# Performance work log

Hardware: AMD Instinct MI355X
Metric: run time of the kernel (lower is better)

The kernel has to match this reference:

```python
import jax, jax.numpy as jnp
import numpy as np

N = 100000   # nodes
E = 1600000  # edges (before self loops)
D = 128      # input_dim
H1 = 128     # hidden_dim_1
H2 = 128     # hidden_dim_2
OUT = 1      # output_dim
G = 64       # number of graphs in the batch


def setup_inputs() -> dict:
    key = jax.random.key(0)
    ks = jax.random.split(key, 11)
    x = jax.random.normal(ks[0], (N, D), dtype=jnp.float32)
    edge_index = jax.random.randint(ks[1], (2, E), 0, N, dtype=jnp.int64)
    batch = jnp.sort(jax.random.randint(ks[2], (N,), 0, G, dtype=jnp.int64))
    s = 0.05
    W1 = jax.random.normal(ks[3], (D, H1), dtype=jnp.float32) * s
    b1 = jnp.zeros((H1,), dtype=jnp.float32)
    W2 = jax.random.normal(ks[4], (H1, H2), dtype=jnp.float32) * s
    b2 = jnp.zeros((H2,), dtype=jnp.float32)
    W_iou = jax.random.normal(ks[5], (H2, OUT), dtype=jnp.float32) * s
    b_iou = jnp.zeros((OUT,), dtype=jnp.float32)
    W_iop = jax.random.normal(ks[6], (H2, OUT), dtype=jnp.float32) * s
    b_iop = jnp.zeros((OUT,), dtype=jnp.float32)
    return dict(x=x, edge_index=edge_index, batch=batch,
                W1=W1, b1=b1, W2=W2, b2=b2,
                W_iou=W_iou, b_iou=b_iou, W_iop=W_iop, b_iop=b_iop)


def reference(x, edge_index, batch, W1, b1, W2, b2, W_iou, b_iou, W_iop, b_iop):
    n = x.shape[0]
    # add_self_loops
    loops = jnp.arange(n, dtype=edge_index.dtype)
    src = jnp.concatenate([edge_index[0], loops])
    dst = jnp.concatenate([edge_index[1], loops])
    # symmetric GCN normalization: deg over target nodes
    deg = jax.ops.segment_sum(jnp.ones_like(dst, dtype=x.dtype), dst, num_segments=n)
    dinv = jnp.where(deg > 0, jax.lax.rsqrt(deg), 0.0)
    norm = dinv[src] * dinv[dst]  # [E+N]

    def gcn_conv(h, W, b):
        hw = h @ W                                  # [N, H]
        m = hw[src] * norm[:, None]                 # gather + normalize [E+N, H]
        return jax.ops.segment_sum(m, dst, num_segments=n) + b  # scatter-add

    h = jax.nn.relu(gcn_conv(x, W1, b1))
    h = jax.nn.relu(gcn_conv(h, W2, b2))
    # global_max_pool over graph ids
    pooled = jax.ops.segment_max(h, batch, num_segments=G)
    pooled = jnp.where(jnp.isfinite(pooled), pooled, 0.0)  # guard empty graphs
    iou = pooled @ W_iou + b_iou
    iop = pooled @ W_iop + b_iop
    return jnp.concatenate([iou, iop], axis=1)  # [G, 2*OUT]
```

## Files before the change

kernel.cpp:

```cpp
#include <hip/hip_runtime.h>
#include <math.h>

typedef unsigned int u32;
typedef __attribute__((ext_vector_type(8))) short short8v;
typedef __attribute__((ext_vector_type(4))) float floatx4;

__device__ inline int rfl(int v) { return __builtin_amdgcn_readfirstlane(v); }

__device__ inline float blo(u32 u) { return __uint_as_float(u << 16); }
__device__ inline float bhi(u32 u) { return __uint_as_float(u & 0xffff0000u); }
__device__ inline u32 f2b(float f) {
    u32 u = __float_as_uint(f);
    return (u + 0x7fffu + ((u >> 16) & 1u)) >> 16;
}
__device__ inline u32 pack2(float a, float b) { return f2b(a) | (f2b(b) << 16); }

#define FILL_EPT 16
__global__ __launch_bounds__(256) void bfill_k(const int* __restrict__ src, const int* __restrict__ dst,
                                               u32* __restrict__ gcursor, u32* __restrict__ pairs,
                                               int E, int B, int CAP) {
    __shared__ u32 lcnt[256];
    __shared__ u32 lbase[256];
    const int t = threadIdx.x;
    lcnt[t] = 0;
    __syncthreads();

    const int base_e = blockIdx.x * (256 * FILL_EPT);
    u32 pk[FILL_EPT];
    u32 bk[FILL_EPT];
    u32 rk[FILL_EPT];
#pragma unroll
    for (int q = 0; q < FILL_EPT / 4; ++q) {
        int e0 = base_e + (q * 256 + t) * 4;
        if (e0 + 3 < E) {
            int4 s4 = *(const int4*)(src + e0);
            int4 d4 = *(const int4*)(dst + e0);
            int ss[4] = {s4.x, s4.y, s4.z, s4.w};
            int dd[4] = {d4.x, d4.y, d4.z, d4.w};
#pragma unroll
            for (int r = 0; r < 4; ++r) {
                int j = q * 4 + r;
                u32 b = (u32)dd[r] >> 9;
                pk[j] = (u32)ss[r] | (((u32)dd[r] & 511u) << 17);
                bk[j] = b;
                rk[j] = atomicAdd(&lcnt[b], 1u);
            }
        } else {
#pragma unroll
            for (int r = 0; r < 4; ++r) {
                int j = q * 4 + r;
                int e = e0 + r;
                pk[j] = 0xFFFFFFFFu;
                if (e < E) {
                    int d = dst[e];
                    u32 b = (u32)d >> 9;
                    pk[j] = (u32)src[e] | (((u32)d & 511u) << 17);
                    bk[j] = b;
                    rk[j] = atomicAdd(&lcnt[b], 1u);
                }
            }
        }
    }
    __syncthreads();
    if (t < B) {
        u32 v = lcnt[t];
        lbase[t] = v ? atomicAdd(&gcursor[t], v) : 0u;
    }
    __syncthreads();
#pragma unroll
    for (int j = 0; j < FILL_EPT; ++j) {
        if (pk[j] != 0xFFFFFFFFu) {
            u32 b = bk[j];
            u32 pos = lbase[b] + rk[j];
            if (pos < (u32)CAP) pairs[(size_t)b * CAP + pos] = pk[j];
        }
    }
}

__global__ __launch_bounds__(512) void csort_k(const u32* __restrict__ pairs, const u32* __restrict__ gcursor,
                                               u32* __restrict__ csr, uint2* __restrict__ rowinfo,
                                               float* __restrict__ dinv, int N, int CAP,
                                               const float* __restrict__ W1, const float* __restrict__ W2,
                                               ushort* __restrict__ W1t, ushort* __restrict__ W2t,
                                               u32* __restrict__ pooled) {
    __shared__ u32 hist[512];
    __shared__ u32 scanb[512];
    const int b = blockIdx.x, t = threadIdx.x;
    const u32 base = (u32)b * (u32)CAP;
    u32 cnt = gcursor[b];
    if (cnt > (u32)CAP) cnt = (u32)CAP;

    hist[t] = 0u;
    __syncthreads();
    for (u32 j = t; j < cnt; j += 512) {
        u32 p = pairs[base + j];
        atomicAdd(&hist[p >> 17], 1u);
    }
    __syncthreads();
    u32 v = hist[t];
    scanb[t] = v;
    __syncthreads();
    for (int off = 1; off < 512; off <<= 1) {
        u32 x = (t >= off) ? scanb[t - off] : 0u;
        __syncthreads();
        scanb[t] += x;
        __syncthreads();
    }
    u32 excl_t = scanb[t] - v;

    int i = (b << 9) + t;
    if (i < N) {
        rowinfo[i] = make_uint2(base + excl_t, v);
        dinv[i] = rsqrtf((float)(v + 1u));
    }
    __syncthreads();
    hist[t] = excl_t;
    __syncthreads();
    for (u32 j = t; j < cnt; j += 512) {
        u32 p = pairs[base + j];
        u32 loc = p >> 17;
        u32 pos = atomicAdd(&hist[loc], 1u);
        csr[base + pos] = p & 0x1FFFFu;
    }

    if (b < 32) {
        int idx = b * 512 + t;
        int k = idx >> 7, jj = idx & 127;
        W1t[jj * 128 + k] = (ushort)f2b(W1[idx]);
        W2t[jj * 128 + k] = (ushort)f2b(W2[idx]);
    } else if (b < 48) {
        int idx = (b - 32) * 512 + t;
        pooled[idx] = 0u;
    }
}

__device__ inline int swz(int row, int kbyte) { return row * 256 + (kbyte ^ ((row & 7) << 4)); }

template <bool BF16IN>
__global__ __launch_bounds__(512) void gemm_mfma_k(const void* __restrict__ inp, const ushort* __restrict__ Wt,
                                                   const float* __restrict__ dinv,
                                                   ushort* __restrict__ outp, int N) {
    __shared__ char Wl[128 * 256];
    const int t = threadIdx.x;
    const int brow = blockIdx.x * 256;

    {
        const uint4* g = (const uint4*)Wt;
#pragma unroll
        for (int i = 0; i < 4; ++i) {
            int f = t + i * 512;
            int r = f >> 4, kb = (f & 15) << 4;
            *(uint4*)(Wl + swz(r, kb)) = g[f];
        }
    }

    const int lane = t & 63;
    const int wave = t >> 6;
    const int l15 = lane & 15;
    const int g4 = lane >> 4;

    short8v a[2][4];
#pragma unroll
    for (int mt = 0; mt < 2; ++mt) {
        int row = brow + wave * 32 + mt * 16 + l15;
        bool ok = row < N;
        int rowc = ok ? row : 0;
#pragma unroll
        for (int ks = 0; ks < 4; ++ks) {
            uint4 v = make_uint4(0u, 0u, 0u, 0u);
            if (BF16IN) {
                if (ok) v = *(const uint4*)((const char*)inp + (size_t)rowc * 256 + (ks * 64 + g4 * 16));
            } else {
                if (ok) {
                    const float4* p = (const float4*)((const char*)inp + (size_t)rowc * 512 + (ks * 128 + g4 * 32));
                    float4 x0 = p[0], x1 = p[1];
                    v = make_uint4(pack2(x0.x, x0.y), pack2(x0.z, x0.w), pack2(x1.x, x1.y), pack2(x1.z, x1.w));
                }
            }
            a[mt][ks] = *(short8v*)&v;
        }
    }
    __syncthreads();

    floatx4 acc[2][8];
#pragma unroll
    for (int mt = 0; mt < 2; ++mt)
#pragma unroll
        for (int nt = 0; nt < 8; ++nt) acc[mt][nt] = (floatx4){0.f, 0.f, 0.f, 0.f};

#pragma unroll
    for (int ks = 0; ks < 4; ++ks) {
        int kb = ks * 64 + g4 * 16;
        short8v b[8];
#pragma unroll
        for (int nt = 0; nt < 8; ++nt)
            b[nt] = *(const short8v*)(Wl + swz(nt * 16 + l15, kb));
#pragma unroll
        for (int mt = 0; mt < 2; ++mt)
#pragma unroll
            for (int nt = 0; nt < 8; ++nt)
                acc[mt][nt] = __builtin_amdgcn_mfma_f32_16x16x32_bf16(a[mt][ks], b[nt], acc[mt][nt], 0, 0, 0);
    }

    const int r0w = g4 * 4;
#pragma unroll
    for (int mt = 0; mt < 2; ++mt) {
#pragma unroll
        for (int reg = 0; reg < 4; ++reg) {
            int grow = brow + wave * 32 + mt * 16 + r0w + reg;
            if (grow < N) {
                float sc = dinv[grow];
#pragma unroll
                for (int nt = 0; nt < 8; ++nt)
                    outp[grow * 128 + nt * 16 + l15] = (ushort)f2b(acc[mt][nt][reg] * sc);
            }
        }
    }
}

__device__ inline void edge_row_accum8(const u32* __restrict__ hw, const u32* __restrict__ csr,
                                       int r0, int deg, int lane, float& a0, float& a1) {
    int j = 0;
    for (; j + 8 <= deg; j += 8) {
        int s0 = rfl((int)csr[r0 + j + 0]);
        int s1 = rfl((int)csr[r0 + j + 1]);
        int s2 = rfl((int)csr[r0 + j + 2]);
        int s3 = rfl((int)csr[r0 + j + 3]);
        int s4 = rfl((int)csr[r0 + j + 4]);
        int s5 = rfl((int)csr[r0 + j + 5]);
        int s6 = rfl((int)csr[r0 + j + 6]);
        int s7 = rfl((int)csr[r0 + j + 7]);
        u32 u0 = hw[(size_t)s0 * 64 + lane];
        u32 u1 = hw[(size_t)s1 * 64 + lane];
        u32 u2 = hw[(size_t)s2 * 64 + lane];
        u32 u3 = hw[(size_t)s3 * 64 + lane];
        u32 u4 = hw[(size_t)s4 * 64 + lane];
        u32 u5 = hw[(size_t)s5 * 64 + lane];
        u32 u6 = hw[(size_t)s6 * 64 + lane];
        u32 u7 = hw[(size_t)s7 * 64 + lane];
        a0 += blo(u0); a1 += bhi(u0);
        a0 += blo(u1); a1 += bhi(u1);
        a0 += blo(u2); a1 += bhi(u2);
        a0 += blo(u3); a1 += bhi(u3);
        a0 += blo(u4); a1 += bhi(u4);
        a0 += blo(u5); a1 += bhi(u5);
        a0 += blo(u6); a1 += bhi(u6);
        a0 += blo(u7); a1 += bhi(u7);
    }
    if (j < deg) {
        const int rem = deg - j;
#pragma unroll
        for (int k = 0; k < 8; ++k) {
            int off = (k < rem) ? k : (rem - 1);
            int s = rfl((int)csr[r0 + j + off]);
            u32 u = hw[(size_t)s * 64 + lane];
            float v0 = (k < rem) ? blo(u) : 0.f;
            float v1 = (k < rem) ? bhi(u) : 0.f;
            a0 += v0; a1 += v1;
        }
    }
}

__global__ __launch_bounds__(256) void edge_accum_k(const u32* __restrict__ hw, const uint2* __restrict__ rowinfo,
                                                    const u32* __restrict__ csr, const float* __restrict__ dinv,
                                                    const float* __restrict__ bias, u32* __restrict__ hout, int N) {
    const int lane = threadIdx.x & 63;
    const int wid = (blockIdx.x * blockDim.x + threadIdx.x) >> 6;
    const int nw = (gridDim.x * blockDim.x) >> 6;
    const float2 bb = ((const float2*)bias)[lane];

    for (int i = wid; i < N; i += nw) {
        uint2 ri = rowinfo[i];
        const int r0 = rfl((int)ri.x);
        const int deg = rfl((int)ri.y);
        float di = dinv[i];
        u32 us = hw[(size_t)i * 64 + lane];
        float a0 = blo(us), a1 = bhi(us);

        edge_row_accum8(hw, csr, r0, deg, lane, a0, a1);

        a0 = fmaxf(fmaf(a0, di, bb.x), 0.f);
        a1 = fmaxf(fmaf(a1, di, bb.y), 0.f);
        hout[(size_t)i * 64 + lane] = pack2(a0, a1);
    }
}

__global__ __launch_bounds__(256) void edge_pool_k(const u32* __restrict__ hw, const uint2* __restrict__ rowinfo,
                                                   const u32* __restrict__ csr, const float* __restrict__ dinv,
                                                   const float* __restrict__ bias, const int* __restrict__ batch,
                                                   u32* __restrict__ pooled, int N, int chunk) {
    const int lane = threadIdx.x & 63;
    const int gwid = (blockIdx.x * blockDim.x + threadIdx.x) >> 6;
    const float2 bb = ((const float2*)bias)[lane];

    int i0 = gwid * chunk, i1 = min(N, i0 + chunk);
    float m0 = 0.f, m1 = 0.f;
    int gcur = -1;
    for (int i = i0; i < i1; ++i) {
        uint2 ri = rowinfo[i];
        const int r0 = rfl((int)ri.x);
        const int deg = rfl((int)ri.y);
        float di = dinv[i];
        u32 us = hw[(size_t)i * 64 + lane];
        float a0 = blo(us), a1 = bhi(us);

        edge_row_accum8(hw, csr, r0, deg, lane, a0, a1);

        a0 = fmaxf(fmaf(a0, di, bb.x), 0.f);
        a1 = fmaxf(fmaf(a1, di, bb.y), 0.f);

        int g = batch[i];
        if (g != gcur) {
            if (gcur >= 0) {
                atomicMax(pooled + gcur * 128 + lane * 2,     __float_as_uint(m0));
                atomicMax(pooled + gcur * 128 + lane * 2 + 1, __float_as_uint(m1));
            }
            gcur = g;
            m0 = m1 = 0.f;
        }
        m0 = fmaxf(m0, a0);
        m1 = fmaxf(m1, a1);
    }
    if (gcur >= 0) {
        atomicMax(pooled + gcur * 128 + lane * 2,     __float_as_uint(m0));
        atomicMax(pooled + gcur * 128 + lane * 2 + 1, __float_as_uint(m1));
    }
}

__global__ void final_k(const float* __restrict__ pooled, const float* __restrict__ Wu, const float* __restrict__ bu,
                        const float* __restrict__ Wp, const float* __restrict__ bp, float* __restrict__ out) {
    int t = threadIdx.x;
    int g = t >> 1, c = t & 1;
    const float* w = c ? Wp : Wu;
    const float* pr = pooled + g * 128;
    float s = 0.f;
    for (int k = 0; k < 128; k += 4)
        s += pr[k] * w[k] + pr[k + 1] * w[k + 1] + pr[k + 2] * w[k + 2] + pr[k + 3] * w[k + 3];
    out[g * 2 + c] = s + (c ? bp[0] : bu[0]);
}

extern "C" void kernel_launch(void* const* d_in, const int* in_sizes, int n_in,
                              void* d_out, int out_size, void* d_ws, size_t ws_size,
                              hipStream_t stream) {
    const float* x     = (const float*)d_in[0];
    const int*   ei    = (const int*)d_in[1];
    const int*   batch = (const int*)d_in[2];
    const float* W1    = (const float*)d_in[3];
    const float* b1    = (const float*)d_in[4];
    const float* W2    = (const float*)d_in[5];
    const float* b2    = (const float*)d_in[6];
    const float* Wu    = (const float*)d_in[7];
    const float* bu    = (const float*)d_in[8];
    const float* Wp    = (const float*)d_in[9];
    const float* bp    = (const float*)d_in[10];
    float* out = (float*)d_out;

    const int N = in_sizes[2];
    const int E = in_sizes[1] / 2;
    const int* src = ei;
    const int* dst = ei + E;

    const int B = (N + 511) >> 9;
    int avg = E / B;
    int CAP = avg + 6 * (int)sqrt((double)avg) + 64;
    CAP = (CAP + 63) & ~63;

    char* ws = (char*)d_ws;
    size_t o = 0;
    auto alloc = [&](size_t bytes) { size_t r = o; o += (bytes + 255) & ~(size_t)255; return r; };
    u32*   gcursor = (u32*)(ws + alloc(1024));
    float* dinv    = (float*)(ws + alloc((size_t)N * 4));
    uint2* rowinfo = (uint2*)(ws + alloc((size_t)N * 8));
    u32*   csr     = (u32*)(ws + alloc((size_t)B * CAP * 4));
    ushort* hwA    = (ushort*)(ws + alloc((size_t)N * 128 * 2));
    ushort* hwB    = (ushort*)(ws + alloc((size_t)N * 128 * 2));
    u32*   pooled  = (u32*)(ws + alloc(64 * 128 * 4));
    ushort* W1t    = (ushort*)(ws + alloc(128 * 128 * 2));
    ushort* W2t    = (ushort*)(ws + alloc(128 * 128 * 2));
    u32*   pairs   = (u32*)hwA;
    (void)ws_size; (void)n_in;

    const int gFill = (E + 256 * FILL_EPT - 1) / (256 * FILL_EPT);
    const int gGemm = (N + 255) / 256;
    const int nWaves = 2048 * 4;
    const int chunk = (N + nWaves - 1) / nWaves;

    hipMemsetAsync(gcursor, 0, 1024, stream);
    bfill_k<<<gFill, 256, 0, stream>>>(src, dst, gcursor, pairs, E, B, CAP);
    csort_k<<<B, 512, 0, stream>>>(pairs, gcursor, csr, rowinfo, dinv, N, CAP, W1, W2, W1t, W2t, pooled);

    gemm_mfma_k<false><<<gGemm, 512, 0, stream>>>((const void*)x, W1t, dinv, hwA, N);
    edge_accum_k<<<2048, 256, 0, stream>>>((const u32*)hwA, rowinfo, csr, dinv, b1, (u32*)hwB, N);
    gemm_mfma_k<true><<<gGemm, 512, 0, stream>>>((const void*)hwB, W2t, dinv, hwA, N);
    edge_pool_k<<<2048, 256, 0, stream>>>((const u32*)hwA, rowinfo, csr, dinv, b2, batch, pooled, N, chunk);

    final_k<<<1, 128, 0, stream>>>((const float*)pooled, Wu, bu, Wp, bp, out);
}
```

Measured before the change: 200.9 us.

## Store hidden features in feature-sliced layout and gather per slice

The GEMM output is now stored as 8 column slices of 16 bf16 features, each slice contiguous across nodes. The edge aggregation kernels assign each block one slice, with 8 nodes per wave and 8 lanes per node, so each gathered neighbor read is 32 bytes from a 3.2 MB slice. The aim is better cache locality for random neighbor gathers, since each slice can stay resident in cache. In exchange, every node's CSR list is re-read 8 times, lanes with different degrees diverge within a wave, and the second GEMM's input loads become strided.

```diff
diff --git a/kernel.cpp b/kernel.cpp
--- a/kernel.cpp
+++ b/kernel.cpp
@@ -143,6 +143,7 @@
     __shared__ char Wl[128 * 256];
     const int t = threadIdx.x;
     const int brow = blockIdx.x * 256;
+    const size_t NS = (size_t)N * 16;
 
     {
         const uint4* g = (const uint4*)Wt;
@@ -169,7 +170,10 @@
         for (int ks = 0; ks < 4; ++ks) {
             uint4 v = make_uint4(0u, 0u, 0u, 0u);
             if (BF16IN) {
-                if (ok) v = *(const uint4*)((const char*)inp + (size_t)rowc * 256 + (ks * 64 + g4 * 16));
+                if (ok) {
+                    int sl = 2 * ks + (g4 >> 1);
+                    v = *(const uint4*)((const char*)inp + (size_t)sl * NS * 2 + (size_t)rowc * 32 + (g4 & 1) * 16);
+                }
             } else {
                 if (ok) {
                     const float4* p = (const float4*)((const char*)inp + (size_t)rowc * 512 + (ks * 128 + g4 * 32));
@@ -212,118 +216,80 @@
                 float sc = dinv[grow];
 #pragma unroll
                 for (int nt = 0; nt < 8; ++nt)
-                    outp[grow * 128 + nt * 16 + l15] = (ushort)f2b(acc[mt][nt][reg] * sc);
-            }
-        }
-    }
-}
-
-__device__ inline void edge_row_accum8(const u32* __restrict__ hw, const u32* __restrict__ csr,
-                                       int r0, int deg, int lane, float& a0, float& a1) {
-    int j = 0;
-    for (; j + 8 <= deg; j += 8) {
-        int s0 = rfl((int)csr[r0 + j + 0]);
-        int s1 = rfl((int)csr[r0 + j + 1]);
-        int s2 = rfl((int)csr[r0 + j + 2]);
-        int s3 = rfl((int)csr[r0 + j + 3]);
-        int s4 = rfl((int)csr[r0 + j + 4]);
-        int s5 = rfl((int)csr[r0 + j + 5]);
-        int s6 = rfl((int)csr[r0 + j + 6]);
-        int s7 = rfl((int)csr[r0 + j + 7]);
-        u32 u0 = hw[(size_t)s0 * 64 + lane];
-        u32 u1 = hw[(size_t)s1 * 64 + lane];
-        u32 u2 = hw[(size_t)s2 * 64 + lane];
-        u32 u3 = hw[(size_t)s3 * 64 + lane];
-        u32 u4 = hw[(size_t)s4 * 64 + lane];
-        u32 u5 = hw[(size_t)s5 * 64 + lane];
-        u32 u6 = hw[(size_t)s6 * 64 + lane];
-        u32 u7 = hw[(size_t)s7 * 64 + lane];
-        a0 += blo(u0); a1 += bhi(u0);
-        a0 += blo(u1); a1 += bhi(u1);
-        a0 += blo(u2); a1 += bhi(u2);
-        a0 += blo(u3); a1 += bhi(u3);
-        a0 += blo(u4); a1 += bhi(u4);
-        a0 += blo(u5); a1 += bhi(u5);
-        a0 += blo(u6); a1 += bhi(u6);
-        a0 += blo(u7); a1 += bhi(u7);
-    }
-    if (j < deg) {
-        const int rem = deg - j;
-#pragma unroll
-        for (int k = 0; k < 8; ++k) {
-            int off = (k < rem) ? k : (rem - 1);
-            int s = rfl((int)csr[r0 + j + off]);
-            u32 u = hw[(size_t)s * 64 + lane];
-            float v0 = (k < rem) ? blo(u) : 0.f;
-            float v1 = (k < rem) ? bhi(u) : 0.f;
-            a0 += v0; a1 += v1;
-        }
-    }
-}
-
-__global__ __launch_bounds__(256) void edge_accum_k(const u32* __restrict__ hw, const uint2* __restrict__ rowinfo,
-                                                    const u32* __restrict__ csr, const float* __restrict__ dinv,
-                                                    const float* __restrict__ bias, u32* __restrict__ hout, int N) {
-    const int lane = threadIdx.x & 63;
-    const int wid = (blockIdx.x * blockDim.x + threadIdx.x) >> 6;
-    const int nw = (gridDim.x * blockDim.x) >> 6;
-    const float2 bb = ((const float2*)bias)[lane];
-
-    for (int i = wid; i < N; i += nw) {
-        uint2 ri = rowinfo[i];
-        const int r0 = rfl((int)ri.x);
-        const int deg = rfl((int)ri.y);
-        float di = dinv[i];
-        u32 us = hw[(size_t)i * 64 + lane];
-        float a0 = blo(us), a1 = bhi(us);
-
-        edge_row_accum8(hw, csr, r0, deg, lane, a0, a1);
-
-        a0 = fmaxf(fmaf(a0, di, bb.x), 0.f);
-        a1 = fmaxf(fmaf(a1, di, bb.y), 0.f);
-        hout[(size_t)i * 64 + lane] = pack2(a0, a1);
-    }
-}
-
-__global__ __launch_bounds__(256) void edge_pool_k(const u32* __restrict__ hw, const uint2* __restrict__ rowinfo,
-                                                   const u32* __restrict__ csr, const float* __restrict__ dinv,
-                                                   const float* __restrict__ bias, const int* __restrict__ batch,
-                                                   u32* __restrict__ pooled, int N, int chunk) {
-    const int lane = threadIdx.x & 63;
-    const int gwid = (blockIdx.x * blockDim.x + threadIdx.x) >> 6;
-    const float2 bb = ((const float2*)bias)[lane];
-
-    int i0 = gwid * chunk, i1 = min(N, i0 + chunk);
+                    outp[(size_t)nt * NS + (size_t)grow * 16 + l15] = (ushort)f2b(acc[mt][nt][reg] * sc);
+            }
+        }
+    }
+}
+
+template <int MODE>
+__global__ __launch_bounds__(256) void edge_sliced_k(const u32* __restrict__ hw, const uint2* __restrict__ rowinfo,
+                                                     const u32* __restrict__ csr, const float* __restrict__ dinv,
+                                                     const float* __restrict__ bias, const int* __restrict__ batch,
+                                                     u32* __restrict__ outbuf, u32* __restrict__ pooled,
+                                                     int N, int gpw) {
+    const int t = threadIdx.x;
+    const int lane = t & 63;
+    const int slice = blockIdx.x & 7;
+    const int wv = (blockIdx.x >> 3) * 4 + (t >> 6);
+    const int sg = lane >> 3;
+    const int d = lane & 7;
+    const size_t N8 = (size_t)N * 8;
+    const u32* hws = hw + (size_t)slice * N8;
+    const float2 bb = ((const float2*)bias)[slice * 8 + d];
+
     float m0 = 0.f, m1 = 0.f;
     int gcur = -1;
-    for (int i = i0; i < i1; ++i) {
-        uint2 ri = rowinfo[i];
-        const int r0 = rfl((int)ri.x);
-        const int deg = rfl((int)ri.y);
-        float di = dinv[i];
-        u32 us = hw[(size_t)i * 64 + lane];
-        float a0 = blo(us), a1 = bhi(us);
-
-        edge_row_accum8(hw, csr, r0, deg, lane, a0, a1);
-
-        a0 = fmaxf(fmaf(a0, di, bb.x), 0.f);
-        a1 = fmaxf(fmaf(a1, di, bb.y), 0.f);
-
-        int g = batch[i];
-        if (g != gcur) {
-            if (gcur >= 0) {
-                atomicMax(pooled + gcur * 128 + lane * 2,     __float_as_uint(m0));
-                atomicMax(pooled + gcur * 128 + lane * 2 + 1, __float_as_uint(m1));
-            }
-            gcur = g;
-            m0 = m1 = 0.f;
-        }
-        m0 = fmaxf(m0, a0);
-        m1 = fmaxf(m1, a1);
-    }
-    if (gcur >= 0) {
-        atomicMax(pooled + gcur * 128 + lane * 2,     __float_as_uint(m0));
-        atomicMax(pooled + gcur * 128 + lane * 2 + 1, __float_as_uint(m1));
+    const int g0 = wv * gpw;
+    for (int gi = 0; gi < gpw; ++gi) {
+        int i = (g0 + gi) * 8 + sg;
+        if (i < N) {
+            uint2 ri = rowinfo[i];
+            int r0 = (int)ri.x;
+            int deg = (int)ri.y;
+            float di = dinv[i];
+            u32 us = hws[(size_t)i * 8 + d];
+            float a0 = blo(us), a1 = bhi(us);
+
+            int degm1 = (deg > 0) ? (deg - 1) : 0;
+            int j = 0;
+            while (__ballot(j < deg)) {
+#pragma unroll
+                for (int k = 0; k < 4; ++k) {
+                    int jk = j + k;
+                    int jj = (jk < degm1) ? jk : degm1;
+                    u32 sid = __builtin_nontemporal_load(csr + r0 + jj);
+                    u32 u = hws[(size_t)sid * 8 + d];
+                    bool valid = jk < deg;
+                    a0 += valid ? blo(u) : 0.f;
+                    a1 += valid ? bhi(u) : 0.f;
+                }
+                j += 4;
+            }
+
+            a0 = fmaxf(fmaf(a0, di, bb.x), 0.f);
+            a1 = fmaxf(fmaf(a1, di, bb.y), 0.f);
+
+            if constexpr (MODE == 0) {
+                outbuf[(size_t)slice * N8 + (size_t)i * 8 + d] = pack2(a0, a1);
+            } else {
+                int g = batch[i];
+                if (g != gcur) {
+                    if (gcur >= 0) {
+                        atomicMax(pooled + gcur * 128 + slice * 16 + d * 2,     __float_as_uint(m0));
+                        atomicMax(pooled + gcur * 128 + slice * 16 + d * 2 + 1, __float_as_uint(m1));
+                    }
+                    gcur = g;
+                    m0 = m1 = 0.f;
+                }
+                m0 = fmaxf(m0, a0);
+                m1 = fmaxf(m1, a1);
+            }
+        }
+    }
+    if (MODE == 1 && gcur >= 0) {
+        atomicMax(pooled + gcur * 128 + slice * 16 + d * 2,     __float_as_uint(m0));
+        atomicMax(pooled + gcur * 128 + slice * 16 + d * 2 + 1, __float_as_uint(m1));
     }
 }
 
@@ -382,17 +348,19 @@
 
     const int gFill = (E + 256 * FILL_EPT - 1) / (256 * FILL_EPT);
     const int gGemm = (N + 255) / 256;
-    const int nWaves = 2048 * 4;
-    const int chunk = (N + nWaves - 1) / nWaves;
+    const int ngroups = (N + 7) / 8;
+    const int gpw = (ngroups + 1023) / 1024;
 
     hipMemsetAsync(gcursor, 0, 1024, stream);
     bfill_k<<<gFill, 256, 0, stream>>>(src, dst, gcursor, pairs, E, B, CAP);
     csort_k<<<B, 512, 0, stream>>>(pairs, gcursor, csr, rowinfo, dinv, N, CAP, W1, W2, W1t, W2t, pooled);
 
     gemm_mfma_k<false><<<gGemm, 512, 0, stream>>>((const void*)x, W1t, dinv, hwA, N);
-    edge_accum_k<<<2048, 256, 0, stream>>>((const u32*)hwA, rowinfo, csr, dinv, b1, (u32*)hwB, N);
+    edge_sliced_k<0><<<2048, 256, 0, stream>>>((const u32*)hwA, rowinfo, csr, dinv, b1, batch,
+                                               (u32*)hwB, nullptr, N, gpw);
     gemm_mfma_k<true><<<gGemm, 512, 0, stream>>>((const void*)hwB, W2t, dinv, hwA, N);
-    edge_pool_k<<<2048, 256, 0, stream>>>((const u32*)hwA, rowinfo, csr, dinv, b2, batch, pooled, N, chunk);
+    edge_sliced_k<1><<<2048, 256, 0, stream>>>((const u32*)hwA, rowinfo, csr, dinv, b2, batch,
+                                               nullptr, pooled, N, gpw);
 
     final_k<<<1, 128, 0, stream>>>((const float*)pooled, Wu, bu, Wp, bp, out);
 }
```

After: 624.9 us. 211% more time.

## Fuse first GEMM into CSR sort kernel by deferring source-degree scaling

Applied to the files above, without the earlier changes.

The first-layer X·W1 GEMM no longer needs dinv, so it now runs in the same grid as the CSR counting sort: extra blocks past B do the GEMM while the sort blocks build the CSR. To allow this, the first edge aggregation applies dinv[src] per gathered neighbor instead of pre-scaling rows. The weight transpose and pooled zeroing move into the bucket fill kernel, and the pairs buffer moves to hwB so it does not overlap the GEMM output. This removes one launch and lets the GEMM overlap the sort, at the cost of an extra dinv gather per edge in the first aggregation.

```diff
diff --git a/kernel.cpp b/kernel.cpp
--- a/kernel.cpp
+++ b/kernel.cpp
@@ -18,12 +18,27 @@
 #define FILL_EPT 16
 __global__ __launch_bounds__(256) void bfill_k(const int* __restrict__ src, const int* __restrict__ dst,
                                                u32* __restrict__ gcursor, u32* __restrict__ pairs,
-                                               int E, int B, int CAP) {
+                                               int E, int B, int CAP,
+                                               const float* __restrict__ W1, const float* __restrict__ W2,
+                                               ushort* __restrict__ W1t, ushort* __restrict__ W2t,
+                                               u32* __restrict__ pooled) {
     __shared__ u32 lcnt[256];
     __shared__ u32 lbase[256];
     const int t = threadIdx.x;
     lcnt[t] = 0;
     __syncthreads();
+
+    {
+        const int b = blockIdx.x;
+        if (b < 64) {
+            int idx = b * 256 + t;
+            int k = idx >> 7, jj = idx & 127;
+            W1t[jj * 128 + k] = (ushort)f2b(W1[idx]);
+            W2t[jj * 128 + k] = (ushort)f2b(W2[idx]);
+        } else if (b < 96) {
+            pooled[(b - 64) * 256 + t] = 0u;
+        }
+    }
 
     const int base_e = blockIdx.x * (256 * FILL_EPT);
     u32 pk[FILL_EPT];
@@ -77,73 +92,12 @@
     }
 }
 
-__global__ __launch_bounds__(512) void csort_k(const u32* __restrict__ pairs, const u32* __restrict__ gcursor,
-                                               u32* __restrict__ csr, uint2* __restrict__ rowinfo,
-                                               float* __restrict__ dinv, int N, int CAP,
-                                               const float* __restrict__ W1, const float* __restrict__ W2,
-                                               ushort* __restrict__ W1t, ushort* __restrict__ W2t,
-                                               u32* __restrict__ pooled) {
-    __shared__ u32 hist[512];
-    __shared__ u32 scanb[512];
-    const int b = blockIdx.x, t = threadIdx.x;
-    const u32 base = (u32)b * (u32)CAP;
-    u32 cnt = gcursor[b];
-    if (cnt > (u32)CAP) cnt = (u32)CAP;
-
-    hist[t] = 0u;
-    __syncthreads();
-    for (u32 j = t; j < cnt; j += 512) {
-        u32 p = pairs[base + j];
-        atomicAdd(&hist[p >> 17], 1u);
-    }
-    __syncthreads();
-    u32 v = hist[t];
-    scanb[t] = v;
-    __syncthreads();
-    for (int off = 1; off < 512; off <<= 1) {
-        u32 x = (t >= off) ? scanb[t - off] : 0u;
-        __syncthreads();
-        scanb[t] += x;
-        __syncthreads();
-    }
-    u32 excl_t = scanb[t] - v;
-
-    int i = (b << 9) + t;
-    if (i < N) {
-        rowinfo[i] = make_uint2(base + excl_t, v);
-        dinv[i] = rsqrtf((float)(v + 1u));
-    }
-    __syncthreads();
-    hist[t] = excl_t;
-    __syncthreads();
-    for (u32 j = t; j < cnt; j += 512) {
-        u32 p = pairs[base + j];
-        u32 loc = p >> 17;
-        u32 pos = atomicAdd(&hist[loc], 1u);
-        csr[base + pos] = p & 0x1FFFFu;
-    }
-
-    if (b < 32) {
-        int idx = b * 512 + t;
-        int k = idx >> 7, jj = idx & 127;
-        W1t[jj * 128 + k] = (ushort)f2b(W1[idx]);
-        W2t[jj * 128 + k] = (ushort)f2b(W2[idx]);
-    } else if (b < 48) {
-        int idx = (b - 32) * 512 + t;
-        pooled[idx] = 0u;
-    }
-}
-
 __device__ inline int swz(int row, int kbyte) { return row * 256 + (kbyte ^ ((row & 7) << 4)); }
 
-template <bool BF16IN>
-__global__ __launch_bounds__(512) void gemm_mfma_k(const void* __restrict__ inp, const ushort* __restrict__ Wt,
-                                                   const float* __restrict__ dinv,
-                                                   ushort* __restrict__ outp, int N) {
-    __shared__ char Wl[128 * 256];
-    const int t = threadIdx.x;
-    const int brow = blockIdx.x * 256;
-
+template <bool BF16IN, bool SCALE>
+__device__ __forceinline__ void gemm_body(const void* __restrict__ inp, const ushort* __restrict__ Wt,
+                                          const float* __restrict__ dinv, ushort* __restrict__ outp,
+                                          int N, int brow, char* Wl, int t) {
     {
         const uint4* g = (const uint4*)Wt;
 #pragma unroll
@@ -209,7 +163,7 @@
         for (int reg = 0; reg < 4; ++reg) {
             int grow = brow + wave * 32 + mt * 16 + r0w + reg;
             if (grow < N) {
-                float sc = dinv[grow];
+                float sc = SCALE ? dinv[grow] : 1.f;
 #pragma unroll
                 for (int nt = 0; nt < 8; ++nt)
                     outp[grow * 128 + nt * 16 + l15] = (ushort)f2b(acc[mt][nt][reg] * sc);
@@ -218,8 +172,71 @@
     }
 }
 
-__device__ inline void edge_row_accum8(const u32* __restrict__ hw, const u32* __restrict__ csr,
-                                       int r0, int deg, int lane, float& a0, float& a1) {
+__global__ __launch_bounds__(512) void csort_gemm_k(const u32* __restrict__ pairs, const u32* __restrict__ gcursor,
+                                                    u32* __restrict__ csr, uint2* __restrict__ rowinfo,
+                                                    float* __restrict__ dinv, int N, int CAP, int B,
+                                                    const float* __restrict__ x, const ushort* __restrict__ W1t,
+                                                    ushort* __restrict__ hw1) {
+    __shared__ __align__(16) char smem[32768];
+    const int t = threadIdx.x;
+
+    if (blockIdx.x >= B) {
+        gemm_body<false, false>((const void*)x, W1t, nullptr, hw1, N, (blockIdx.x - B) * 256, smem, t);
+        return;
+    }
+
+    u32* hist = (u32*)smem;
+    u32* scanb = (u32*)(smem + 2048);
+    const int b = blockIdx.x;
+    const u32 base = (u32)b * (u32)CAP;
+    u32 cnt = gcursor[b];
+    if (cnt > (u32)CAP) cnt = (u32)CAP;
+
+    hist[t] = 0u;
+    __syncthreads();
+    for (u32 j = t; j < cnt; j += 512) {
+        u32 p = pairs[base + j];
+        atomicAdd(&hist[p >> 17], 1u);
+    }
+    __syncthreads();
+    u32 v = hist[t];
+    scanb[t] = v;
+    __syncthreads();
+    for (int off = 1; off < 512; off <<= 1) {
+        u32 x2 = (t >= off) ? scanb[t - off] : 0u;
+        __syncthreads();
+        scanb[t] += x2;
+        __syncthreads();
+    }
+    u32 excl_t = scanb[t] - v;
+
+    int i = (b << 9) + t;
+    if (i < N) {
+        rowinfo[i] = make_uint2(base + excl_t, v);
+        dinv[i] = rsqrtf((float)(v + 1u));
+    }
+    __syncthreads();
+    hist[t] = excl_t;
+    __syncthreads();
+    for (u32 j = t; j < cnt; j += 512) {
+        u32 p = pairs[base + j];
+        u32 loc = p >> 17;
+        u32 pos = atomicAdd(&hist[loc], 1u);
+        csr[base + pos] = p & 0x1FFFFu;
+    }
+}
+
+__global__ __launch_bounds__(512) void gemm_mfma_k(const void* __restrict__ inp, const ushort* __restrict__ Wt,
+                                                   const float* __restrict__ dinv,
+                                                   ushort* __restrict__ outp, int N) {
+    __shared__ __align__(16) char Wl[32768];
+    gemm_body<true, true>(inp, Wt, dinv, outp, N, blockIdx.x * 256, Wl, threadIdx.x);
+}
+
+template <bool SCALE>
+__device__ __forceinline__ void edge_row_accum8(const u32* __restrict__ hw, const u32* __restrict__ csr,
+                                                const float* __restrict__ dinv,
+                                                int r0, int deg, int lane, float& a0, float& a1) {
     int j = 0;
     for (; j + 8 <= deg; j += 8) {
         int s0 = rfl((int)csr[r0 + j + 0]);
@@ -230,6 +247,14 @@
         int s5 = rfl((int)csr[r0 + j + 5]);
         int s6 = rfl((int)csr[r0 + j + 6]);
         int s7 = rfl((int)csr[r0 + j + 7]);
+        float w0 = SCALE ? dinv[s0] : 1.f;
+        float w1 = SCALE ? dinv[s1] : 1.f;
+        float w2 = SCALE ? dinv[s2] : 1.f;
+        float w3 = SCALE ? dinv[s3] : 1.f;
+        float w4 = SCALE ? dinv[s4] : 1.f;
+        float w5 = SCALE ? dinv[s5] : 1.f;
+        float w6 = SCALE ? dinv[s6] : 1.f;
+        float w7 = SCALE ? dinv[s7] : 1.f;
         u32 u0 = hw[(size_t)s0 * 64 + lane];
         u32 u1 = hw[(size_t)s1 * 64 + lane];
         u32 u2 = hw[(size_t)s2 * 64 + lane];
@@ -238,14 +263,25 @@
         u32 u5 = hw[(size_t)s5 * 64 + lane];
         u32 u6 = hw[(size_t)s6 * 64 + lane];
         u32 u7 = hw[(size_t)s7 * 64 + lane];
-        a0 += blo(u0); a1 += bhi(u0);
-        a0 += blo(u1); a1 += bhi(u1);
-        a0 += blo(u2); a1 += bhi(u2);
-        a0 += blo(u3); a1 += bhi(u3);
-        a0 += blo(u4); a1 += bhi(u4);
-        a0 += blo(u5); a1 += bhi(u5);
-        a0 += blo(u6); a1 += bhi(u6);
-        a0 += blo(u7); a1 += bhi(u7);
+        if (SCALE) {
+            a0 = fmaf(w0, blo(u0), a0); a1 = fmaf(w0, bhi(u0), a1);
+            a0 = fmaf(w1, blo(u1), a0); a1 = fmaf(w1, bhi(u1), a1);
+            a0 = fmaf(w2, blo(u2), a0); a1 = fmaf(w2, bhi(u2), a1);
+            a0 = fmaf(w3, blo(u3), a0); a1 = fmaf(w3, bhi(u3), a1);
+            a0 = fmaf(w4, blo(u4), a0); a1 = fmaf(w4, bhi(u4), a1);
+            a0 = fmaf(w5, blo(u5), a0); a1 = fmaf(w5, bhi(u5), a1);
+            a0 = fmaf(w6, blo(u6), a0); a1 = fmaf(w6, bhi(u6), a1);
+            a0 = fmaf(w7, blo(u7), a0); a1 = fmaf(w7, bhi(u7), a1);
+        } else {
+            a0 += blo(u0); a1 += bhi(u0);
+            a0 += blo(u1); a1 += bhi(u1);
+            a0 += blo(u2); a1 += bhi(u2);
+            a0 += blo(u3); a1 += bhi(u3);
+            a0 += blo(u4); a1 += bhi(u4);
+            a0 += blo(u5); a1 += bhi(u5);
+            a0 += blo(u6); a1 += bhi(u6);
+            a0 += blo(u7); a1 += bhi(u7);
+        }
     }
     if (j < deg) {
         const int rem = deg - j;
@@ -254,8 +290,10 @@
             int off = (k < rem) ? k : (rem - 1);
             int s = rfl((int)csr[r0 + j + off]);
             u32 u = hw[(size_t)s * 64 + lane];
-            float v0 = (k < rem) ? blo(u) : 0.f;
-            float v1 = (k < rem) ? bhi(u) : 0.f;
+            float w = SCALE ? dinv[s] : 1.f;
+            bool valid = k < rem;
+            float v0 = valid ? w * blo(u) : 0.f;
+            float v1 = valid ? w * bhi(u) : 0.f;
             a0 += v0; a1 += v1;
         }
     }
@@ -275,9 +313,9 @@
         const int deg = rfl((int)ri.y);
         float di = dinv[i];
         u32 us = hw[(size_t)i * 64 + lane];
-        float a0 = blo(us), a1 = bhi(us);
-
-        edge_row_accum8(hw, csr, r0, deg, lane, a0, a1);
+        float a0 = di * blo(us), a1 = di * bhi(us);
+
+        edge_row_accum8<true>(hw, csr, dinv, r0, deg, lane, a0, a1);
 
         a0 = fmaxf(fmaf(a0, di, bb.x), 0.f);
         a1 = fmaxf(fmaf(a1, di, bb.y), 0.f);
@@ -304,7 +342,7 @@
         u32 us = hw[(size_t)i * 64 + lane];
         float a0 = blo(us), a1 = bhi(us);
 
-        edge_row_accum8(hw, csr, r0, deg, lane, a0, a1);
+        edge_row_accum8<false>(hw, csr, nullptr, r0, deg, lane, a0, a1);
 
         a0 = fmaxf(fmaf(a0, di, bb.x), 0.f);
         a1 = fmaxf(fmaf(a1, di, bb.y), 0.f);
@@ -377,7 +415,7 @@
     u32*   pooled  = (u32*)(ws + alloc(64 * 128 * 4));
     ushort* W1t    = (ushort*)(ws + alloc(128 * 128 * 2));
     ushort* W2t    = (ushort*)(ws + alloc(128 * 128 * 2));
-    u32*   pairs   = (u32*)hwA;
+    u32*   pairs   = (u32*)hwB;
     (void)ws_size; (void)n_in;
 
     const int gFill = (E + 256 * FILL_EPT - 1) / (256 * FILL_EPT);
@@ -386,12 +424,11 @@
     const int chunk = (N + nWaves - 1) / nWaves;
 
     hipMemsetAsync(gcursor, 0, 1024, stream);
-    bfill_k<<<gFill, 256, 0, stream>>>(src, dst, gcursor, pairs, E, B, CAP);
-    csort_k<<<B, 512, 0, stream>>>(pairs, gcursor, csr, rowinfo, dinv, N, CAP, W1, W2, W1t, W2t, pooled);
-
-    gemm_mfma_k<false><<<gGemm, 512, 0, stream>>>((const void*)x, W1t, dinv, hwA, N);
+    bfill_k<<<gFill, 256, 0, stream>>>(src, dst, gcursor, pairs, E, B, CAP, W1, W2, W1t, W2t, pooled);
+    csort_gemm_k<<<B + gGemm, 512, 0, stream>>>(pairs, gcursor, csr, rowinfo, dinv, N, CAP, B, x, W1t, hwA);
+
     edge_accum_k<<<2048, 256, 0, stream>>>((const u32*)hwA, rowinfo, csr, dinv, b1, (u32*)hwB, N);
-    gemm_mfma_k<true><<<gGemm, 512, 0, stream>>>((const void*)hwB, W2t, dinv, hwA, N);
+    gemm_mfma_k<<<gGemm, 512, 0, stream>>>((const void*)hwB, W2t, dinv, hwA, N);
     edge_pool_k<<<2048, 256, 0, stream>>>((const u32*)hwA, rowinfo, csr, dinv, b2, batch, pooled, N, chunk);
 
     final_k<<<1, 128, 0, stream>>>((const float*)pooled, Wu, bu, Wp, bp, out);
```

Result: no change. 200.5 us (-0.2%).
